# Kernel optimization log

Measured on AMD Instinct MI355X. Metric: run time of the kernel, lower is better.

## Reference

```python
import jax, jax.numpy as jnp
import numpy as np

N_NODES = 50000
N_EDGES = 300000
IN_CH = 128
HIDDEN = 64
OUT_CH = 40
NUM_LAYERS = 4
HEADS = 8


def setup_inputs() -> dict:
    key = jax.random.key(0)
    ks = jax.random.split(key, 8)
    s = lambda fan_in: 1.0 / np.sqrt(fan_in)
    return {
        "x": jax.random.normal(ks[0], (N_NODES, IN_CH), dtype=jnp.float32),
        "edge_index": jax.random.randint(ks[1], (2, N_EDGES), 0, N_NODES, dtype=jnp.int64),
        "heads": HEADS,
        "w1": jax.random.uniform(ks[2], (IN_CH, HIDDEN), jnp.float32, -s(IN_CH), s(IN_CH)),
        "b1": jnp.zeros((HIDDEN,), jnp.float32),
        "wq": jax.random.uniform(ks[3], (NUM_LAYERS, HIDDEN, HIDDEN), jnp.float32, -s(HIDDEN), s(HIDDEN)),
        "wk": jax.random.uniform(ks[4], (NUM_LAYERS, HIDDEN, HIDDEN), jnp.float32, -s(HIDDEN), s(HIDDEN)),
        "wv": jax.random.uniform(ks[5], (NUM_LAYERS, HIDDEN, HIDDEN), jnp.float32, -s(HIDDEN), s(HIDDEN)),
        "w2": jax.random.uniform(ks[6], (HIDDEN, OUT_CH), jnp.float32, -s(HIDDEN), s(HIDDEN)),
        "b2": jnp.zeros((OUT_CH,), jnp.float32),
    }


def _dna_conv(x_all, src, dst, norm, wq, wk, wv, heads):
    # x_all: [N, L, C]; attention of each node's latest state over neighbors' full history.
    N, L, C = x_all.shape
    d = C // heads
    q = (x_all[:, -1] @ wq).reshape(N, heads, d)      # [N, h, d]
    k = (x_all @ wk).reshape(N, L, heads, d)          # [N, L, h, d]
    v = (x_all @ wv).reshape(N, L, heads, d)
    qe = q[dst]                                       # [E, h, d]
    ke = k[src]                                       # [E, L, h, d]
    ve = v[src]
    scale = 1.0 / jnp.sqrt(jnp.asarray(d, x_all.dtype))
    score = jnp.einsum('ehd,elhd->ehl', qe, ke) * scale
    attn = jax.nn.softmax(score, axis=-1)             # softmax over history L
    msg = jnp.einsum('ehl,elhd->ehd', attn, ve).reshape(-1, C)
    msg = msg * norm[:, None]                         # GCN symmetric norm per edge
    return jax.ops.segment_sum(msg, dst, num_segments=N)  # sum-aggregate at target


def reference(x, edge_index, heads, w1, b1, wq, wk, wv, w2, b2):
    N = x.shape[0]
    loop = jnp.arange(N, dtype=edge_index.dtype)
    src = jnp.concatenate([edge_index[0], loop])      # gcn_norm adds self loops
    dst = jnp.concatenate([edge_index[1], loop])
    ew = jnp.ones(src.shape[0], x.dtype)
    deg = jax.ops.segment_sum(ew, dst, num_segments=N)
    dinv = jnp.where(deg > 0, jax.lax.rsqrt(deg), 0.0)
    norm = dinv[src] * dinv[dst]

    h = jax.nn.relu(x @ w1 + b1)                      # lin1 + ReLU (DFALayer = identity fwd)
    x_all = h[:, None, :]                             # [N, 1, C]
    for i in range(wq.shape[0]):
        out = jax.nn.relu(_dna_conv(x_all, src, dst, norm, wq[i], wk[i], wv[i], heads))
        x_all = jnp.concatenate([x_all, out[:, None, :]], axis=1)
    logits = x_all[:, -1] @ w2 + b2
    return jax.nn.log_softmax(logits, axis=1)
```

## Files before the change

### kernel.cpp

```cpp
#include <hip/hip_runtime.h>
#include <hip/hip_fp16.h>
#include <math.h>

#define N_NODES 50000
#define N_EDGES 300000
#define E_TOT (N_EDGES + N_NODES)
#define IN_CH 128
#define HIDDEN 64
#define OUT_CH 40
#define NUM_LAYERS 4
#define NCHUNK ((N_NODES + 255) / 256)
#define NTILES (N_NODES / 16)
#define QKV_WPR 512

typedef _Float16 h8 __attribute__((ext_vector_type(8)));
typedef float f32x4 __attribute__((ext_vector_type(4)));

#define MFMA16(a, b, c) __builtin_amdgcn_mfma_f32_16x16x32_f16((a), (b), (c), 0, 0, 0)

__global__ void k_count_init(int* count, int* fill) {
    int n = blockIdx.x * blockDim.x + threadIdx.x;
    if (n < N_NODES) { count[n] = 1; fill[n] = 1; }
}

__global__ void k_count(const int* __restrict__ dst, int* count) {
    int e = blockIdx.x * blockDim.x + threadIdx.x;
    if (e < N_EDGES) atomicAdd(&count[dst[e]], 1);
}

__global__ __launch_bounds__(256) void k_scan_a(const int* __restrict__ count,
                                                int* __restrict__ loc,
                                                int* __restrict__ psum) {
    __shared__ int s[256];
    int tid = threadIdx.x;
    int g = blockIdx.x * 256 + tid;
    int v = (g < N_NODES) ? count[g] : 0;
    s[tid] = v;
    __syncthreads();
    for (int off = 1; off < 256; off <<= 1) {
        int t = (tid >= off) ? s[tid - off] : 0;
        __syncthreads();
        s[tid] += t;
        __syncthreads();
    }
    if (g < N_NODES) loc[g] = s[tid] - v;
    if (tid == 255) psum[blockIdx.x] = s[255];
}

__global__ __launch_bounds__(256) void k_scan_b(int* psum) {
    __shared__ int s[256];
    int tid = threadIdx.x;
    int v = (tid < NCHUNK) ? psum[tid] : 0;
    s[tid] = v;
    __syncthreads();
    for (int off = 1; off < 256; off <<= 1) {
        int t = (tid >= off) ? s[tid - off] : 0;
        __syncthreads();
        s[tid] += t;
        __syncthreads();
    }
    if (tid < NCHUNK) psum[tid] = s[tid] - v;
}

__global__ void k_scan_c(const int* __restrict__ count, const int* __restrict__ loc,
                         const int* __restrict__ psum, int* __restrict__ rowptr,
                         float* __restrict__ dinv, int2* __restrict__ edata) {
    int n = blockIdx.x * blockDim.x + threadIdx.x;
    if (n >= N_NODES) return;
    int rp = loc[n] + psum[n >> 8];
    rowptr[n] = rp;
    float di = rsqrtf((float)count[n]);
    dinv[n] = di;
    edata[rp] = make_int2(n, __float_as_int(di * di));
    if (n == 0) rowptr[N_NODES] = E_TOT;
}

__global__ void k_scatter(const int* __restrict__ ei, const int* __restrict__ rowptr,
                          int* __restrict__ fill, const float* __restrict__ dinv,
                          int2* __restrict__ edata) {
    int e = blockIdx.x * blockDim.x + threadIdx.x;
    if (e >= N_EDGES) return;
    int s = ei[e], d = ei[N_EDGES + e];
    int p = rowptr[d] + atomicAdd(&fill[d], 1);
    edata[p] = make_int2(s, __float_as_int(dinv[s] * dinv[d]));
}

__device__ __forceinline__ h8 load_bfrag(const float* __restrict__ W, int ncols,
                                         int kbase, int c) {
    h8 r;
#pragma unroll
    for (int i = 0; i < 8; ++i) r[i] = (_Float16)W[(kbase + i) * ncols + c];
    return r;
}

__device__ __forceinline__ void unpack8(float4 raw, float* f) {
    const __half2* hp = (const __half2*)&raw;
#pragma unroll
    for (int i = 0; i < 4; ++i) {
        float2 t = __half22float2(hp[i]);
        f[2 * i] = t.x;
        f[2 * i + 1] = t.y;
    }
}

__device__ __forceinline__ float2 pack4(float a, float b, float c, float d) {
    union { __half2 h2[2]; float2 f2; } u;
    u.h2[0] = __floats2half2_rn(a, b);
    u.h2[1] = __floats2half2_rn(c, d);
    return u.f2;
}

__global__ __launch_bounds__(256) void k_h_mfma(const float* __restrict__ x,
                                                const float* __restrict__ w1,
                                                const float* __restrict__ b1,
                                                __half* __restrict__ xh) {
    int lane = threadIdx.x & 63;
    int gw = blockIdx.x * 4 + (threadIdx.x >> 6);
    int krow = lane >> 4, col = lane & 15;
    h8 B[4][4];
#pragma unroll
    for (int ct = 0; ct < 4; ++ct)
#pragma unroll
        for (int s = 0; s < 4; ++s)
            B[ct][s] = load_bfrag(w1, HIDDEN, krow * 8 + 32 * s, ct * 16 + col);
    float4 bias[4];
#pragma unroll
    for (int ct = 0; ct < 4; ++ct) bias[ct] = *(const float4*)&b1[ct * 16 + krow * 4];
    for (int t = gw; t < NTILES; t += 1024) {
        int n0 = t * 16;
        const float* xrow = x + (size_t)(n0 + col) * IN_CH + krow * 8;
        f32x4 acc[4] = {{0.f, 0.f, 0.f, 0.f}, {0.f, 0.f, 0.f, 0.f},
                        {0.f, 0.f, 0.f, 0.f}, {0.f, 0.f, 0.f, 0.f}};
#pragma unroll
        for (int s = 0; s < 4; ++s) {
            float4 p0 = *(const float4*)(xrow + 32 * s);
            float4 p1 = *(const float4*)(xrow + 32 * s + 4);
            h8 a;
            a[0] = (_Float16)p0.x; a[1] = (_Float16)p0.y;
            a[2] = (_Float16)p0.z; a[3] = (_Float16)p0.w;
            a[4] = (_Float16)p1.x; a[5] = (_Float16)p1.y;
            a[6] = (_Float16)p1.z; a[7] = (_Float16)p1.w;
#pragma unroll
            for (int ct = 0; ct < 4; ++ct) acc[ct] = MFMA16(B[ct][s], a, acc[ct]);
        }
        __half* op = xh + (size_t)(n0 + col) * 320 + krow * 4;
#pragma unroll
        for (int ct = 0; ct < 4; ++ct) {
            float2 pk = pack4(fmaxf(acc[ct][0] + bias[ct].x, 0.f),
                              fmaxf(acc[ct][1] + bias[ct].y, 0.f),
                              fmaxf(acc[ct][2] + bias[ct].z, 0.f),
                              fmaxf(acc[ct][3] + bias[ct].w, 0.f));
            *(float2*)(op + ct * 16) = pk;
        }
    }
}

__global__ __launch_bounds__(256) void k_v1_mfma(const __half* __restrict__ xh,
                                                 const float* __restrict__ wv,
                                                 __half* __restrict__ vh1) {
    int lane = threadIdx.x & 63;
    int gw = blockIdx.x * 4 + (threadIdx.x >> 6);
    int krow = lane >> 4, col = lane & 15;
    h8 B[4][2];
#pragma unroll
    for (int ct = 0; ct < 4; ++ct)
#pragma unroll
        for (int s = 0; s < 2; ++s)
            B[ct][s] = load_bfrag(wv, HIDDEN, krow * 8 + 32 * s, ct * 16 + col);
    for (int t = gw; t < NTILES; t += QKV_WPR) {
        int n0 = t * 16;
        const __half* ap = xh + (size_t)(n0 + col) * 320 + krow * 8;
        h8 a0 = *(const h8*)(const void*)ap;
        h8 a1 = *(const h8*)(const void*)(ap + 32);
        f32x4 acc[4] = {{0.f, 0.f, 0.f, 0.f}, {0.f, 0.f, 0.f, 0.f},
                        {0.f, 0.f, 0.f, 0.f}, {0.f, 0.f, 0.f, 0.f}};
#pragma unroll
        for (int ct = 0; ct < 4; ++ct) {
            acc[ct] = MFMA16(B[ct][0], a0, acc[ct]);
            acc[ct] = MFMA16(B[ct][1], a1, acc[ct]);
        }
        __half* op = vh1 + (size_t)(n0 + col) * 64 + krow * 4;
#pragma unroll
        for (int ct = 0; ct < 4; ++ct)
            *(float2*)(op + ct * 16) =
                pack4(acc[ct][0], acc[ct][1], acc[ct][2], acc[ct][3]);
    }
}

__global__ __launch_bounds__(256) void k_edge_l1(const int* __restrict__ rowptr,
                                                 const int2* __restrict__ edata,
                                                 const __half* __restrict__ vh1,
                                                 __half* __restrict__ xh) {
    int tid = threadIdx.x;
    int wid = tid >> 6, lane = tid & 63;
    int g = lane >> 3, r = lane & 7;
    int d = blockIdx.x * 4 + wid;
    if (d >= N_NODES) return;
    int rs = rowptr[d], re = rowptr[d + 1];
    float acc[8];
#pragma unroll
    for (int i = 0; i < 8; ++i) acc[i] = 0.f;
    for (int base = rs; base < re; base += 8) {
        int eidx = base + g;
        bool valid = eidx < re;
        int2 e = edata[valid ? eidx : rs];
        int s = e.x;
        float nrm = valid ? __int_as_float(e.y) : 0.f;
        float4 raw = *(const float4*)(vh1 + (size_t)s * 64 + r * 8);
        float f[8];
        unpack8(raw, f);
#pragma unroll
        for (int c = 0; c < 8; ++c) acc[c] = fmaf(nrm, f[c], acc[c]);
    }
#pragma unroll
    for (int c = 0; c < 8; ++c) {
        acc[c] += __shfl_xor(acc[c], 8);
        acc[c] += __shfl_xor(acc[c], 16);
        acc[c] += __shfl_xor(acc[c], 32);
    }
    if (lane < 8) {
        __half hbuf[8];
#pragma unroll
        for (int c = 0; c < 8; ++c) hbuf[c] = __float2half(fmaxf(acc[c], 0.f));
        *(float4*)(xh + (size_t)d * 320 + 64 + r * 8) = *(float4*)hbuf;
    }
}

template <int L>
__global__ __launch_bounds__(256) void k_qkv_mfma(const __half* __restrict__ xh,
                                                  const float* __restrict__ wq,
                                                  const float* __restrict__ wk,
                                                  const float* __restrict__ wv,
                                                  __half* __restrict__ qh,
                                                  __half* __restrict__ kvi) {
    int lane = threadIdx.x & 63;
    int gw = blockIdx.x * 4 + (threadIdx.x >> 6);
    int role = gw / QKV_WPR;
    int slot = gw - role * QKV_WPR;
    int krow = lane >> 4, col = lane & 15;
    if (role == 0) {
        int lx = L - 1;
        h8 B[4][2];
#pragma unroll
        for (int ct = 0; ct < 4; ++ct)
#pragma unroll
            for (int s = 0; s < 2; ++s)
                B[ct][s] = load_bfrag(wq, HIDDEN, krow * 8 + 32 * s, ct * 16 + col);
        for (int t = slot; t < NTILES; t += QKV_WPR) {
            int n0 = t * 16;
            const __half* ap = xh + (size_t)(n0 + col) * 320 + lx * 64 + krow * 8;
            h8 a0 = *(const h8*)(const void*)ap;
            h8 a1 = *(const h8*)(const void*)(ap + 32);
            f32x4 acc[4] = {{0.f, 0.f, 0.f, 0.f}, {0.f, 0.f, 0.f, 0.f},
                            {0.f, 0.f, 0.f, 0.f}, {0.f, 0.f, 0.f, 0.f}};
#pragma unroll
            for (int ct = 0; ct < 4; ++ct) {
                acc[ct] = MFMA16(B[ct][0], a0, acc[ct]);
                acc[ct] = MFMA16(B[ct][1], a1, acc[ct]);
            }
            const float scl = 0.35355339059327373f;
            __half* op = qh + (size_t)(n0 + col) * 64 + krow * 4;
#pragma unroll
            for (int ct = 0; ct < 4; ++ct)
                *(float2*)(op + ct * 16) = pack4(acc[ct][0] * scl, acc[ct][1] * scl,
                                                 acc[ct][2] * scl, acc[ct][3] * scl);
        }
    } else {
        int lx = role - 1;
        h8 Bk[4][2], Bv[4][2];
#pragma unroll
        for (int ct = 0; ct < 4; ++ct)
#pragma unroll
            for (int s = 0; s < 2; ++s) {
                Bk[ct][s] = load_bfrag(wk, HIDDEN, krow * 8 + 32 * s, ct * 16 + col);
                Bv[ct][s] = load_bfrag(wv, HIDDEN, krow * 8 + 32 * s, ct * 16 + col);
            }
        for (int t = slot; t < NTILES; t += QKV_WPR) {
            int n0 = t * 16;
            const __half* ap = xh + (size_t)(n0 + col) * 320 + lx * 64 + krow * 8;
            h8 a0 = *(const h8*)(const void*)ap;
            h8 a1 = *(const h8*)(const void*)(ap + 32);
            f32x4 ak[4] = {{0.f, 0.f, 0.f, 0.f}, {0.f, 0.f, 0.f, 0.f},
                           {0.f, 0.f, 0.f, 0.f}, {0.f, 0.f, 0.f, 0.f}};
            f32x4 av[4] = {{0.f, 0.f, 0.f, 0.f}, {0.f, 0.f, 0.f, 0.f},
                           {0.f, 0.f, 0.f, 0.f}, {0.f, 0.f, 0.f, 0.f}};
#pragma unroll
            for (int ct = 0; ct < 4; ++ct) {
                ak[ct] = MFMA16(Bk[ct][0], a0, ak[ct]);
                ak[ct] = MFMA16(Bk[ct][1], a1, ak[ct]);
                av[ct] = MFMA16(Bv[ct][0], a0, av[ct]);
                av[ct] = MFMA16(Bv[ct][1], a1, av[ct]);
            }
            __half* op = kvi + ((size_t)(n0 + col) * L + lx) * 128 + krow * 4;
#pragma unroll
            for (int ct = 0; ct < 4; ++ct) {
                *(float2*)(op + ct * 16) =
                    pack4(ak[ct][0], ak[ct][1], ak[ct][2], ak[ct][3]);
                *(float2*)(op + 64 + ct * 16) =
                    pack4(av[ct][0], av[ct][1], av[ct][2], av[ct][3]);
            }
        }
    }
}

template <int L>
__global__ __launch_bounds__(256) void k_edge_csr8(const int* __restrict__ rowptr,
                                                   const int2* __restrict__ edata,
                                                   const __half* __restrict__ kvi,
                                                   const __half* __restrict__ qh,
                                                   float* __restrict__ aggout,
                                                   __half* __restrict__ xh) {
    int tid = threadIdx.x;
    int wid = tid >> 6, lane = tid & 63;
    int g = lane >> 3, r = lane & 7;
    int d = blockIdx.x * 4 + wid;
    if (d >= N_NODES) return;
    int rs = rowptr[d], re = rowptr[d + 1];
    float qf[8];
    unpack8(((const float4*)(qh + (size_t)d * 64))[r], qf);
    float acc[8];
#pragma unroll
    for (int i = 0; i < 8; ++i) acc[i] = 0.f;
    for (int base = rs; base < re; base += 8) {
        int eidx = base + g;
        bool valid = eidx < re;
        int2 e = edata[valid ? eidx : rs];
        int s = e.x;
        float nrm = valid ? __int_as_float(e.y) : 0.f;
        float sc[L];
        float4 vraw[L];
        const __half* kb = kvi + (size_t)s * (L * 128) + r * 8;
#pragma unroll
        for (int l = 0; l < L; ++l) {
            float4 kraw = *(const float4*)(kb + l * 128);
            vraw[l] = *(const float4*)(kb + l * 128 + 64);
            float kf[8];
            unpack8(kraw, kf);
            float p = 0.f;
#pragma unroll
            for (int c = 0; c < 8; ++c) p = fmaf(qf[c], kf[c], p);
            sc[l] = p;
        }
        float m = sc[0];
#pragma unroll
        for (int l = 1; l < L; ++l) m = fmaxf(m, sc[l]);
        float ssum = 0.f;
#pragma unroll
        for (int l = 0; l < L; ++l) { sc[l] = __expf(sc[l] - m); ssum += sc[l]; }
        float w = __fdividef(nrm, ssum);
#pragma unroll
        for (int l = 0; l < L; ++l) {
            float swl = sc[l] * w;
            float vf[8];
            unpack8(vraw[l], vf);
#pragma unroll
            for (int c = 0; c < 8; ++c) acc[c] = fmaf(swl, vf[c], acc[c]);
        }
    }
#pragma unroll
    for (int c = 0; c < 8; ++c) {
        acc[c] += __shfl_xor(acc[c], 8);
        acc[c] += __shfl_xor(acc[c], 16);
        acc[c] += __shfl_xor(acc[c], 32);
    }
    if (lane < 8) {
        if (L == NUM_LAYERS) {
            float4 o0, o1;
            o0.x = fmaxf(acc[0], 0.f); o0.y = fmaxf(acc[1], 0.f);
            o0.z = fmaxf(acc[2], 0.f); o0.w = fmaxf(acc[3], 0.f);
            o1.x = fmaxf(acc[4], 0.f); o1.y = fmaxf(acc[5], 0.f);
            o1.z = fmaxf(acc[6], 0.f); o1.w = fmaxf(acc[7], 0.f);
            float4* op = (float4*)(aggout + (size_t)d * 64 + r * 8);
            op[0] = o0; op[1] = o1;
        } else {
            __half hbuf[8];
#pragma unroll
            for (int c = 0; c < 8; ++c) hbuf[c] = __float2half(fmaxf(acc[c], 0.f));
            *(float4*)(xh + (size_t)d * 320 + L * 64 + r * 8) = *(float4*)hbuf;
        }
    }
}

__global__ __launch_bounds__(256) void k_final_lds(const float* __restrict__ aggout,
                                                   const float* __restrict__ w2,
                                                   const float* __restrict__ b2,
                                                   float* __restrict__ out) {
    __shared__ float rows[16][HIDDEN];
    int tid = threadIdx.x, wid = tid >> 6, lane = tid & 63;
    int cl = (lane < OUT_CH) ? lane : (OUT_CH - 1);
    float wcol[HIDDEN];
#pragma unroll
    for (int j = 0; j < HIDDEN; ++j) wcol[j] = w2[j * OUT_CH + cl];
    float b = b2[cl];
    for (int t = blockIdx.x; t < NTILES; t += gridDim.x) {
        int n0 = t * 16;
        {
            int rr = tid >> 4, seg = tid & 15;
            *(float4*)&rows[rr][seg * 4] =
                *(const float4*)&aggout[(size_t)(n0 + rr) * 64 + seg * 4];
        }
        __syncthreads();
#pragma unroll
        for (int u = 0; u < 4; ++u) {
            int ln = wid * 4 + u;
            const float4* rp = (const float4*)rows[ln];
            float a0 = 0.f, a1 = 0.f, a2 = 0.f, a3 = 0.f;
#pragma unroll
            for (int jc = 0; jc < HIDDEN / 4; ++jc) {
                float4 r = rp[jc];
                a0 = fmaf(r.x, wcol[jc * 4 + 0], a0);
                a1 = fmaf(r.y, wcol[jc * 4 + 1], a1);
                a2 = fmaf(r.z, wcol[jc * 4 + 2], a2);
                a3 = fmaf(r.w, wcol[jc * 4 + 3], a3);
            }
            float logit = (lane < OUT_CH) ? ((a0 + a1) + (a2 + a3) + b) : -INFINITY;
            float m = logit;
            for (int mask = 32; mask; mask >>= 1) m = fmaxf(m, __shfl_xor(m, mask));
            float ex = (lane < OUT_CH) ? __expf(logit - m) : 0.f;
            float ssum = ex;
            for (int mask = 32; mask; mask >>= 1) ssum += __shfl_xor(ssum, mask);
            if (lane < OUT_CH)
                out[(size_t)(n0 + ln) * OUT_CH + lane] = logit - m - logf(ssum);
        }
        __syncthreads();
    }
}

extern "C" void kernel_launch(void* const* d_in, const int* in_sizes, int n_in,
                              void* d_out, int out_size, void* d_ws, size_t ws_size,
                              hipStream_t stream) {
    const float* x  = (const float*)d_in[0];
    const int*   ei = (const int*)d_in[1];
    const float* w1 = (const float*)d_in[3];
    const float* b1 = (const float*)d_in[4];
    const float* wq = (const float*)d_in[5];
    const float* wk = (const float*)d_in[6];
    const float* wv = (const float*)d_in[7];
    const float* w2 = (const float*)d_in[8];
    const float* b2 = (const float*)d_in[9];
    float* out = (float*)d_out;

    char* cur = (char*)d_ws;
    auto alloc = [&](size_t bytes) { char* p = cur; cur += (bytes + 255) & ~(size_t)255; return p; };
    float*   dinv   = (float*)alloc(N_NODES * 4);
    __half*  xh     = (__half*)alloc((size_t)N_NODES * 320 * 2);
    float*   aggout = (float*)alloc((size_t)N_NODES * 64 * 4);
    __half*  qh     = (__half*)alloc((size_t)N_NODES * 64 * 2);
    __half*  kvi    = (__half*)alloc((size_t)N_NODES * NUM_LAYERS * 128 * 2);
    __half*  vh1    = (__half*)alloc((size_t)N_NODES * 64 * 2);
    int*     count  = (int*)alloc(N_NODES * 4);
    int*     loc    = (int*)alloc(N_NODES * 4);
    int*     psum   = (int*)alloc(256 * 4);
    int*     rowptr = (int*)alloc((N_NODES + 1) * 4);
    int*     fill   = (int*)alloc(N_NODES * 4);
    int2*    edata  = (int2*)alloc((size_t)E_TOT * 8);

    k_count_init<<<(N_NODES + 255) / 256, 256, 0, stream>>>(count, fill);
    k_count<<<(N_EDGES + 255) / 256, 256, 0, stream>>>(ei + N_EDGES, count);
    k_scan_a<<<NCHUNK, 256, 0, stream>>>(count, loc, psum);
    k_scan_b<<<1, 256, 0, stream>>>(psum);
    k_scan_c<<<(N_NODES + 255) / 256, 256, 0, stream>>>(count, loc, psum, rowptr,
                                                        dinv, edata);
    k_scatter<<<(N_EDGES + 255) / 256, 256, 0, stream>>>(ei, rowptr, fill, dinv, edata);

    k_h_mfma<<<256, 256, 0, stream>>>(x, w1, b1, xh);

    k_v1_mfma<<<QKV_WPR / 4, 256, 0, stream>>>(xh, wv, vh1);
    k_edge_l1<<<(N_NODES + 3) / 4, 256, 0, stream>>>(rowptr, edata, vh1, xh);

    for (int i = 1; i < NUM_LAYERS; ++i) {
        int L = i + 1;
        int qkvblk = (L + 1) * (QKV_WPR / 4);
        const float* wqi = wq + i * 4096;
        const float* wki = wk + i * 4096;
        const float* wvi = wv + i * 4096;
        switch (L) {
            case 2:
                k_qkv_mfma<2><<<qkvblk, 256, 0, stream>>>(xh, wqi, wki, wvi, qh, kvi);
                k_edge_csr8<2><<<(N_NODES + 3) / 4, 256, 0, stream>>>(rowptr, edata, kvi, qh, aggout, xh);
                break;
            case 3:
                k_qkv_mfma<3><<<qkvblk, 256, 0, stream>>>(xh, wqi, wki, wvi, qh, kvi);
                k_edge_csr8<3><<<(N_NODES + 3) / 4, 256, 0, stream>>>(rowptr, edata, kvi, qh, aggout, xh);
                break;
            default:
                k_qkv_mfma<4><<<qkvblk, 256, 0, stream>>>(xh, wqi, wki, wvi, qh, kvi);
                k_edge_csr8<4><<<(N_NODES + 3) / 4, 256, 0, stream>>>(rowptr, edata, kvi, qh, aggout, xh);
                break;
        }
    }
    k_final_lds<<<512, 256, 0, stream>>>(aggout, w2, b2, out);
}
```

Before: 287.9 us.

## Store K/V history in FP8 and fuse Q projection into last-layer K/V warps

The per-node K/V history buffer is now stored as FP8 (one byte per element) instead of FP16, so the per-edge gathers in the edge attention kernel read half as many bytes. Unpacking uses the hardware packed FP8-to-F32 conversion builtins. The QKV kernel also merges the separate Q-role warps into the warps handling the latest history slice, reusing the loaded A fragments and launching fewer blocks. FP8 K/V lowers precision and may break the accuracy tolerance.

```diff
diff --git a/kernel.cpp b/kernel.cpp
--- a/kernel.cpp
+++ b/kernel.cpp
@@ -15,6 +15,7 @@
 
 typedef _Float16 h8 __attribute__((ext_vector_type(8)));
 typedef float f32x4 __attribute__((ext_vector_type(4)));
+typedef float f32x2 __attribute__((ext_vector_type(2)));
 
 #define MFMA16(a, b, c) __builtin_amdgcn_mfma_f32_16x16x32_f16((a), (b), (c), 0, 0, 0)
 
@@ -103,6 +104,20 @@
     }
 }
 
+__device__ __forceinline__ void unpack8_fp8(uint2 raw, float* f) {
+    f32x2 t;
+    t = __builtin_amdgcn_cvt_pk_f32_fp8(raw.x, false); f[0] = t[0]; f[1] = t[1];
+    t = __builtin_amdgcn_cvt_pk_f32_fp8(raw.x, true);  f[2] = t[0]; f[3] = t[1];
+    t = __builtin_amdgcn_cvt_pk_f32_fp8(raw.y, false); f[4] = t[0]; f[5] = t[1];
+    t = __builtin_amdgcn_cvt_pk_f32_fp8(raw.y, true);  f[6] = t[0]; f[7] = t[1];
+}
+
+__device__ __forceinline__ int pack4_fp8(float a, float b, float c, float d) {
+    int r = __builtin_amdgcn_cvt_pk_fp8_f32(a, b, 0, false);
+    r = __builtin_amdgcn_cvt_pk_fp8_f32(c, d, r, true);
+    return r;
+}
+
 __device__ __forceinline__ float2 pack4(float a, float b, float c, float d) {
     union { __half2 h2[2]; float2 f2; } u;
     u.h2[0] = __floats2half2_rn(a, b);
@@ -232,73 +247,64 @@
                                                   const float* __restrict__ wk,
                                                   const float* __restrict__ wv,
                                                   __half* __restrict__ qh,
-                                                  __half* __restrict__ kvi) {
+                                                  unsigned char* __restrict__ kvi) {
     int lane = threadIdx.x & 63;
     int gw = blockIdx.x * 4 + (threadIdx.x >> 6);
-    int role = gw / QKV_WPR;
-    int slot = gw - role * QKV_WPR;
+    int lx = gw / QKV_WPR;
+    int slot = gw - lx * QKV_WPR;
     int krow = lane >> 4, col = lane & 15;
-    if (role == 0) {
-        int lx = L - 1;
-        h8 B[4][2];
+    bool doq = (lx == L - 1);
+    h8 Bk[4][2], Bv[4][2], Bq[4][2];
+#pragma unroll
+    for (int ct = 0; ct < 4; ++ct)
+#pragma unroll
+        for (int s = 0; s < 2; ++s) {
+            Bk[ct][s] = load_bfrag(wk, HIDDEN, krow * 8 + 32 * s, ct * 16 + col);
+            Bv[ct][s] = load_bfrag(wv, HIDDEN, krow * 8 + 32 * s, ct * 16 + col);
+        }
+    if (doq) {
 #pragma unroll
         for (int ct = 0; ct < 4; ++ct)
 #pragma unroll
             for (int s = 0; s < 2; ++s)
-                B[ct][s] = load_bfrag(wq, HIDDEN, krow * 8 + 32 * s, ct * 16 + col);
-        for (int t = slot; t < NTILES; t += QKV_WPR) {
-            int n0 = t * 16;
-            const __half* ap = xh + (size_t)(n0 + col) * 320 + lx * 64 + krow * 8;
-            h8 a0 = *(const h8*)(const void*)ap;
-            h8 a1 = *(const h8*)(const void*)(ap + 32);
-            f32x4 acc[4] = {{0.f, 0.f, 0.f, 0.f}, {0.f, 0.f, 0.f, 0.f},
-                            {0.f, 0.f, 0.f, 0.f}, {0.f, 0.f, 0.f, 0.f}};
+                Bq[ct][s] = load_bfrag(wq, HIDDEN, krow * 8 + 32 * s, ct * 16 + col);
+    }
+    for (int t = slot; t < NTILES; t += QKV_WPR) {
+        int n0 = t * 16;
+        const __half* ap = xh + (size_t)(n0 + col) * 320 + lx * 64 + krow * 8;
+        h8 a0 = *(const h8*)(const void*)ap;
+        h8 a1 = *(const h8*)(const void*)(ap + 32);
+        f32x4 ak[4] = {{0.f, 0.f, 0.f, 0.f}, {0.f, 0.f, 0.f, 0.f},
+                       {0.f, 0.f, 0.f, 0.f}, {0.f, 0.f, 0.f, 0.f}};
+        f32x4 av[4] = {{0.f, 0.f, 0.f, 0.f}, {0.f, 0.f, 0.f, 0.f},
+                       {0.f, 0.f, 0.f, 0.f}, {0.f, 0.f, 0.f, 0.f}};
+#pragma unroll
+        for (int ct = 0; ct < 4; ++ct) {
+            ak[ct] = MFMA16(Bk[ct][0], a0, ak[ct]);
+            ak[ct] = MFMA16(Bk[ct][1], a1, ak[ct]);
+            av[ct] = MFMA16(Bv[ct][0], a0, av[ct]);
+            av[ct] = MFMA16(Bv[ct][1], a1, av[ct]);
+        }
+        unsigned char* op = kvi + ((size_t)(n0 + col) * L + lx) * 128 + krow * 4;
+#pragma unroll
+        for (int ct = 0; ct < 4; ++ct) {
+            *(int*)(op + ct * 16) = pack4_fp8(ak[ct][0], ak[ct][1], ak[ct][2], ak[ct][3]);
+            *(int*)(op + 64 + ct * 16) = pack4_fp8(av[ct][0], av[ct][1], av[ct][2], av[ct][3]);
+        }
+        if (doq) {
+            f32x4 aq[4] = {{0.f, 0.f, 0.f, 0.f}, {0.f, 0.f, 0.f, 0.f},
+                           {0.f, 0.f, 0.f, 0.f}, {0.f, 0.f, 0.f, 0.f}};
 #pragma unroll
             for (int ct = 0; ct < 4; ++ct) {
-                acc[ct] = MFMA16(B[ct][0], a0, acc[ct]);
-                acc[ct] = MFMA16(B[ct][1], a1, acc[ct]);
+                aq[ct] = MFMA16(Bq[ct][0], a0, aq[ct]);
+                aq[ct] = MFMA16(Bq[ct][1], a1, aq[ct]);
             }
             const float scl = 0.35355339059327373f;
-            __half* op = qh + (size_t)(n0 + col) * 64 + krow * 4;
+            __half* qp = qh + (size_t)(n0 + col) * 64 + krow * 4;
 #pragma unroll
             for (int ct = 0; ct < 4; ++ct)
-                *(float2*)(op + ct * 16) = pack4(acc[ct][0] * scl, acc[ct][1] * scl,
-                                                 acc[ct][2] * scl, acc[ct][3] * scl);
-        }
-    } else {
-        int lx = role - 1;
-        h8 Bk[4][2], Bv[4][2];
-#pragma unroll
-        for (int ct = 0; ct < 4; ++ct)
-#pragma unroll
-            for (int s = 0; s < 2; ++s) {
-                Bk[ct][s] = load_bfrag(wk, HIDDEN, krow * 8 + 32 * s, ct * 16 + col);
-                Bv[ct][s] = load_bfrag(wv, HIDDEN, krow * 8 + 32 * s, ct * 16 + col);
-            }
-        for (int t = slot; t < NTILES; t += QKV_WPR) {
-            int n0 = t * 16;
-            const __half* ap = xh + (size_t)(n0 + col) * 320 + lx * 64 + krow * 8;
-            h8 a0 = *(const h8*)(const void*)ap;
-            h8 a1 = *(const h8*)(const void*)(ap + 32);
-            f32x4 ak[4] = {{0.f, 0.f, 0.f, 0.f}, {0.f, 0.f, 0.f, 0.f},
-                           {0.f, 0.f, 0.f, 0.f}, {0.f, 0.f, 0.f, 0.f}};
-            f32x4 av[4] = {{0.f, 0.f, 0.f, 0.f}, {0.f, 0.f, 0.f, 0.f},
-                           {0.f, 0.f, 0.f, 0.f}, {0.f, 0.f, 0.f, 0.f}};
-#pragma unroll
-            for (int ct = 0; ct < 4; ++ct) {
-                ak[ct] = MFMA16(Bk[ct][0], a0, ak[ct]);
-                ak[ct] = MFMA16(Bk[ct][1], a1, ak[ct]);
-                av[ct] = MFMA16(Bv[ct][0], a0, av[ct]);
-                av[ct] = MFMA16(Bv[ct][1], a1, av[ct]);
-            }
-            __half* op = kvi + ((size_t)(n0 + col) * L + lx) * 128 + krow * 4;
-#pragma unroll
-            for (int ct = 0; ct < 4; ++ct) {
-                *(float2*)(op + ct * 16) =
-                    pack4(ak[ct][0], ak[ct][1], ak[ct][2], ak[ct][3]);
-                *(float2*)(op + 64 + ct * 16) =
-                    pack4(av[ct][0], av[ct][1], av[ct][2], av[ct][3]);
-            }
+                *(float2*)(qp + ct * 16) = pack4(aq[ct][0] * scl, aq[ct][1] * scl,
+                                                 aq[ct][2] * scl, aq[ct][3] * scl);
         }
     }
 }
@@ -306,7 +312,7 @@
 template <int L>
 __global__ __launch_bounds__(256) void k_edge_csr8(const int* __restrict__ rowptr,
                                                    const int2* __restrict__ edata,
-                                                   const __half* __restrict__ kvi,
+                                                   const unsigned char* __restrict__ kvi,
                                                    const __half* __restrict__ qh,
                                                    float* __restrict__ aggout,
                                                    __half* __restrict__ xh) {
@@ -328,14 +334,14 @@
         int s = e.x;
         float nrm = valid ? __int_as_float(e.y) : 0.f;
         float sc[L];
-        float4 vraw[L];
-        const __half* kb = kvi + (size_t)s * (L * 128) + r * 8;
+        uint2 vraw[L];
+        const unsigned char* kb = kvi + (size_t)s * (L * 128) + r * 8;
 #pragma unroll
         for (int l = 0; l < L; ++l) {
-            float4 kraw = *(const float4*)(kb + l * 128);
-            vraw[l] = *(const float4*)(kb + l * 128 + 64);
+            uint2 kraw = *(const uint2*)(kb + l * 128);
+            vraw[l] = *(const uint2*)(kb + l * 128 + 64);
             float kf[8];
-            unpack8(kraw, kf);
+            unpack8_fp8(kraw, kf);
             float p = 0.f;
 #pragma unroll
             for (int c = 0; c < 8; ++c) p = fmaf(qf[c], kf[c], p);
@@ -352,7 +358,7 @@
         for (int l = 0; l < L; ++l) {
             float swl = sc[l] * w;
             float vf[8];
-            unpack8(vraw[l], vf);
+            unpack8_fp8(vraw[l], vf);
 #pragma unroll
             for (int c = 0; c < 8; ++c) acc[c] = fmaf(swl, vf[c], acc[c]);
         }
@@ -442,18 +448,18 @@
 
     char* cur = (char*)d_ws;
     auto alloc = [&](size_t bytes) { char* p = cur; cur += (bytes + 255) & ~(size_t)255; return p; };
-    float*   dinv   = (float*)alloc(N_NODES * 4);
-    __half*  xh     = (__half*)alloc((size_t)N_NODES * 320 * 2);
-    float*   aggout = (float*)alloc((size_t)N_NODES * 64 * 4);
-    __half*  qh     = (__half*)alloc((size_t)N_NODES * 64 * 2);
-    __half*  kvi    = (__half*)alloc((size_t)N_NODES * NUM_LAYERS * 128 * 2);
-    __half*  vh1    = (__half*)alloc((size_t)N_NODES * 64 * 2);
-    int*     count  = (int*)alloc(N_NODES * 4);
-    int*     loc    = (int*)alloc(N_NODES * 4);
-    int*     psum   = (int*)alloc(256 * 4);
-    int*     rowptr = (int*)alloc((N_NODES + 1) * 4);
-    int*     fill   = (int*)alloc(N_NODES * 4);
-    int2*    edata  = (int2*)alloc((size_t)E_TOT * 8);
+    float*         dinv   = (float*)alloc(N_NODES * 4);
+    __half*        xh     = (__half*)alloc((size_t)N_NODES * 320 * 2);
+    float*         aggout = (float*)alloc((size_t)N_NODES * 64 * 4);
+    __half*        qh     = (__half*)alloc((size_t)N_NODES * 64 * 2);
+    unsigned char* kvi    = (unsigned char*)alloc((size_t)N_NODES * NUM_LAYERS * 128);
+    __half*        vh1    = (__half*)alloc((size_t)N_NODES * 64 * 2);
+    int*           count  = (int*)alloc(N_NODES * 4);
+    int*           loc    = (int*)alloc(N_NODES * 4);
+    int*           psum   = (int*)alloc(256 * 4);
+    int*           rowptr = (int*)alloc((N_NODES + 1) * 4);
+    int*           fill   = (int*)alloc(N_NODES * 4);
+    int2*          edata  = (int2*)alloc((size_t)E_TOT * 8);
 
     k_count_init<<<(N_NODES + 255) / 256, 256, 0, stream>>>(count, fill);
     k_count<<<(N_EDGES + 255) / 256, 256, 0, stream>>>(ei + N_EDGES, count);
@@ -470,7 +476,7 @@
 
     for (int i = 1; i < NUM_LAYERS; ++i) {
         int L = i + 1;
-        int qkvblk = (L + 1) * (QKV_WPR / 4);
+        int qkvblk = L * (QKV_WPR / 4);
         const float* wqi = wq + i * 4096;
         const float* wki = wk + i * 4096;
         const float* wvi = wv + i * 4096;
```

After: 254.7 us. 11.5% less time.
